# Kernel tuning notes

Measured on AMD Instinct MI355X. Metric: run time of the kernel, lower is better.

## Reference

```python
import jax, jax.numpy as jnp
import numpy as np

N_NODES = 20000
IN_CH = 7
HID = 256
HEADS = 8
NEG_SLOPE = 0.2


def glorot(key, shape):
    fan = shape[0] + shape[-1] if len(shape) == 2 else int(np.prod(shape))
    lim = jnp.sqrt(6.0 / fan)
    return jax.random.uniform(key, shape, jnp.float32, -lim, lim)


def setup_inputs() -> dict:
    key = jax.random.key(0)
    ks = jax.random.split(key, 12)
    x = jax.random.normal(ks[0], (N_NODES, IN_CH), jnp.float32)
    edge_index = jax.random.randint(ks[1], (2, 160000), 0, N_NODES, jnp.int64)
    # conv1: in=7 -> heads=8, out=256, concat
    W1 = glorot(ks[2], (IN_CH, HEADS * HID))
    att_src1 = glorot(ks[3], (HEADS, HID))
    att_dst1 = glorot(ks[4], (HEADS, HID))
    b1 = jnp.zeros((HEADS * HID,), jnp.float32)
    # conv2: in=2048 -> heads=1, out=256, mean (concat=False)
    W2 = glorot(ks[5], (HEADS * HID, 1 * HID))
    att_src2 = glorot(ks[6], (1, HID))
    att_dst2 = glorot(ks[7], (1, HID))
    b2 = jnp.zeros((HID,), jnp.float32)
    return {"x": x, "edge_index": edge_index, "W1": W1, "att_src1": att_src1,
            "att_dst1": att_dst1, "b1": b1, "W2": W2, "att_src2": att_src2,
            "att_dst2": att_dst2, "b2": b2}


def gat_conv(x, src, dst, W, att_src, att_dst, bias, concat):
    # PyG GATConv (eval mode, dropout disabled)
    H, C = att_src.shape
    n = x.shape[0]
    h = (x @ W).reshape(n, H, C)                      # [N,H,C]
    a_src = jnp.sum(h * att_src[None], axis=-1)       # [N,H]
    a_dst = jnp.sum(h * att_dst[None], axis=-1)       # [N,H]
    alpha = a_src[src] + a_dst[dst]                   # [E,H]
    alpha = jax.nn.leaky_relu(alpha, NEG_SLOPE)
    # segment softmax over incoming edges of each destination node
    amax = jax.ops.segment_max(alpha, dst, num_segments=n)
    alpha = jnp.exp(alpha - amax[dst])
    denom = jax.ops.segment_sum(alpha, dst, num_segments=n)
    alpha = alpha / (denom[dst] + 1e-16)
    msg = h[src] * alpha[:, :, None]                  # [E,H,C] gather + weight
    out = jax.ops.segment_sum(msg, dst, num_segments=n)  # scatter-add aggregate
    out = out.reshape(n, H * C) if concat else out.mean(axis=1)
    return out + bias


def reference(x, edge_index, W1, att_src1, att_dst1, b1, W2, att_src2, att_dst2, b2):
    n = x.shape[0]
    # PyG GATConv default: add self-loops
    loops = jnp.arange(n, dtype=edge_index.dtype)
    src = jnp.concatenate([edge_index[0], loops])
    dst = jnp.concatenate([edge_index[1], loops])
    h = gat_conv(x, src, dst, W1, att_src1, att_dst1, b1, concat=True)
    h = jax.nn.elu(h)
    out = gat_conv(h, src, dst, W2, att_src2, att_dst2, b2, concat=False)
    return out
```

## Files before the change

kernel.cpp:

```cpp
#include <hip/hip_runtime.h>
#include <hip/hip_bf16.h>

#define N_NODES 20000
#define E_ORIG  160000
#define E_TOT   180000
#define HEADS   8
#define HID     256
#define F1      2048
#define NEG     0.2f
#define MAXDEG  96
#define GBKS    32

typedef __attribute__((ext_vector_type(8))) short  short8;
typedef __attribute__((ext_vector_type(4))) short  short4_;
typedef __attribute__((ext_vector_type(4))) float  f32x4;
typedef __attribute__((ext_vector_type(2))) float  f32x2;

__device__ inline float bf2f(ushort u){ union{unsigned u32; float f;} v; v.u32=((unsigned)u)<<16; return v.f; }
__device__ inline ushort f2bf(float f){
  union{float f; unsigned u;} v; v.f=f;
  unsigned lsb=(v.u>>16)&1u; v.u += 0x7fffu + lsb; return (ushort)(v.u>>16);
}

__device__ inline void gload16(const ushort* g, ushort* s){
  __builtin_amdgcn_global_load_lds((const __attribute__((address_space(1))) unsigned int*)g,
                                   (__attribute__((address_space(3))) unsigned int*)s, 16, 0, 0);
}

__global__ __launch_bounds__(256) void k_pre(const float* __restrict__ x, const float* __restrict__ W1,
    const float* __restrict__ as1, const float* __restrict__ ad1, const float* __restrict__ W2,
    float* __restrict__ a_src1, float* __restrict__ a_dst1, ushort* __restrict__ W2bT,
    int* __restrict__ cnt){
  __shared__ float s_w[128];
  __shared__ ushort sh[256][65];
  int tid = threadIdx.x, bid = blockIdx.x;
  if (tid < 128){
    int t = tid & 63;
    int k = t>>3, i = t&7;
    float v = 0.f;
    if (i < 7){
      const float* wp = W1 + i*F1 + (k<<8);
      const float* ap = ((tid<64) ? as1 : ad1) + (k<<8);
      f32x4 a4 = {0,0,0,0};
      for (int c=0;c<256;c+=4)
        a4 += (*(const f32x4*)&wp[c]) * (*(const f32x4*)&ap[c]);
      v = a4[0]+a4[1]+a4[2]+a4[3];
    }
    s_w[tid] = v;
  }
  __syncthreads();
  {
    int nl = tid>>3, k = tid&7;
    int n = bid*32 + nl;
    if (n < N_NODES){
      float s=0.f, d=0.f;
      const float* ws = &s_w[k*8];
      const float* wd = &s_w[64+k*8];
#pragma unroll
      for (int i=0;i<7;i++){
        float xv = x[n*7+i];
        s += xv*ws[i]; d += xv*wd[i];
      }
      a_src1[n*8+k]=s; a_dst1[n*8+k]=d;
    }
  }
  if (bid >= 32 && bid < 111){
    int i = (bid-32)*256 + tid;
    if (i < N_NODES) cnt[i] = 0;
  }
  if (bid < 32){
    int k0 = bid*64;
    for (int kk=0; kk<64; kk++) sh[tid][kk] = f2bf(W2[(size_t)(k0+kk)*256 + tid]);
    __syncthreads();
#pragma unroll
    for (int c8=0; c8<8; c8++){
      short8 v;
#pragma unroll
      for (int j=0;j<8;j++) v[j] = (short)sh[tid][c8*8+j];
      *(short8*)&W2bT[(size_t)tid*F1 + k0 + c8*8] = v;
    }
  }
}

__global__ void k_scat(const int* __restrict__ ei, int* __restrict__ cnt, int* __restrict__ bucket){
  int e = blockIdx.x*256 + threadIdx.x;
  if (e >= E_TOT) return;
  int s, d;
  if (e < E_ORIG){ s = ei[e]; d = ei[E_ORIG + e]; }
  else           { s = d = e - E_ORIG; }
  int pos = atomicAdd(&cnt[d], 1);
  if (pos < MAXDEG) bucket[d*MAXDEG + pos] = s;
}

__global__ __launch_bounds__(512) void k_sa1(const int* __restrict__ cnt, const int* __restrict__ bucket,
    const float* __restrict__ a_src1, const float* __restrict__ a_dst1,
    const float* __restrict__ x, const float* __restrict__ W1, const float* __restrict__ b1,
    ushort* __restrict__ x2){
  __shared__ float sxa[8][64];
  int tid = threadIdx.x, wv = tid>>6, lane = tid&63;
  int n = blockIdx.x*8 + wv;
  {
    int k = lane>>3, i = lane&7;
    int ie = (i==7)?0:i;
    int base = n*MAXDEG;
    int deg  = cnt[n]; if (deg>MAXDEG) deg=MAXDEG;
    float ad = a_dst1[n*8+k];
    int src0 = (lane<deg)    ? bucket[base+lane]    : 0;
    int src1 = (lane+64<deg) ? bucket[base+lane+64] : 0;
    float denom = 0.f, acc = 0.f;
    int j = 0;
    for (; j+2<=deg; j+=2){
      int s0 = (j<64)   ? __shfl(src0,j)     : __shfl(src1,j-64);
      int s1 = (j+1<64) ? __shfl(src0,j+1)   : __shfl(src1,j-63);
      float A0 = a_src1[(size_t)s0*8+k] + ad;
      float A1 = a_src1[(size_t)s1*8+k] + ad;
      float X0 = x[(size_t)s0*7+ie];
      float X1 = x[(size_t)s1*7+ie];
      A0 = (A0>0.f)?A0:NEG*A0;  A1 = (A1>0.f)?A1:NEG*A1;
      float w0 = __expf(A0),   w1 = __expf(A1);
      denom += w0; acc += w0*X0;
      denom += w1; acc += w1*X1;
    }
    if (j<deg){
      int s0 = (j<64) ? __shfl(src0,j) : __shfl(src1,j-64);
      float A0 = a_src1[(size_t)s0*8+k] + ad;
      A0 = (A0>0.f)?A0:NEG*A0;
      float w0 = __expf(A0);
      denom += w0; acc += w0*x[(size_t)s0*7+ie];
    }
    sxa[wv][lane] = acc/denom;
  }
  __syncthreads();
  int kh = tid>>6, c4 = (tid&63)<<2;
  f32x4 w1r[7];
#pragma unroll
  for (int i=0;i<7;i++) w1r[i] = *(const f32x4*)(W1 + i*F1 + (kh<<8) + c4);
  f32x4 bb = *(const f32x4*)(b1 + (kh<<8) + c4);
#pragma unroll
  for (int g=0; g<8; g++){
    int nn = blockIdx.x*8 + g;
    const float* xa = &sxa[g][kh<<3];
    f32x4 h = bb;
#pragma unroll
    for (int i=0;i<7;i++) h += xa[i]*w1r[i];
    short4_ o;
#pragma unroll
    for (int j=0;j<4;j++){ float v=h[j]; v=(v>0.f)?v:(__expf(v)-1.f); o[j]=(short)f2bf(v); }
    *(short4_*)(x2 + (size_t)nn*F1 + (kh<<8) + c4) = o;
  }
}

__global__ __launch_bounds__(256,3) void k_gemm2m(const ushort* __restrict__ A,
    const ushort* __restrict__ BT, ushort* __restrict__ h2b,
    const float* __restrict__ as2, const float* __restrict__ ad2,
    float* __restrict__ asrc_p, float* __restrict__ adst_p){
  __shared__ __align__(16) ushort S[2][(64+128)*64];
  int tid = threadIdx.x, bid = blockIdx.x;
  int m0 = (bid>>1)*64, n0 = (bid&1)*128, nb = bid&1;
  int w = tid>>6, l = tid&63;
  int lrow = l&15, lk = l>>4;
  int nc = w<<5;

  const ushort* gp[6];
#pragma unroll
  for (int rep=0;rep<6;rep++){
    int lin = rep*256 + tid;
    if (lin < 512){
      int r = lin>>3, s = lin&7;
      int grow = m0 + r; if (grow >= N_NODES) grow = N_NODES-1;
      gp[rep] = A + (size_t)grow*F1 + ((s ^ (r&7))<<3);
    } else {
      int j = lin - 512;
      int c = j>>3, s = j&7;
      gp[rep] = BT + (size_t)(n0+c)*F1 + ((s ^ (c&7))<<3);
    }
  }

  f32x4 acc[4][2] = {};

#pragma unroll
  for (int rep=0;rep<6;rep++) gload16(gp[rep], &S[0][(rep*256+tid)<<3]);
  __syncthreads();

  int cur = 0;
  for (int t=0; t<GBKS; t++){
    if (t+1 < GBKS){
      int k0 = (t+1)<<6;
#pragma unroll
      for (int rep=0;rep<6;rep++) gload16(gp[rep]+k0, &S[cur^1][(rep*256+tid)<<3]);
    }
    const ushort* as_ = &S[cur][0];
    const ushort* bs_ = &S[cur][4096];
#pragma unroll
    for (int kk=0;kk<2;kk++){
      short8 af[4], bfr[2];
#pragma unroll
      for (int m=0;m<4;m++){
        int r = (m<<4) + lrow;
        af[m] = *(const short8*)&as_[(r<<6) + ((((kk<<2)|lk) ^ (r&7))<<3)];
      }
#pragma unroll
      for (int n=0;n<2;n++){
        int c = nc + (n<<4) + lrow;
        bfr[n] = *(const short8*)&bs_[(c<<6) + ((((kk<<2)|lk) ^ (c&7))<<3)];
      }
#pragma unroll
      for (int m=0;m<4;m++)
#pragma unroll
        for (int n=0;n<2;n++)
          acc[m][n] = __builtin_amdgcn_mfma_f32_16x16x32_bf16(af[m], bfr[n], acc[m][n], 0,0,0);
    }
    __syncthreads();
    cur ^= 1;
  }

  float* sps = (float*)&S[0][0];
  float* spd = sps + 256;
  float s2v[2], d2v[2];
#pragma unroll
  for (int n=0;n<2;n++){
    int col = n0 + nc + (n<<4) + lrow;
    s2v[n]=as2[col]; d2v[n]=ad2[col];
  }
#pragma unroll
  for (int m=0;m<4;m++){
#pragma unroll
    for (int j=0;j<4;j++){
      int lr = (m<<4) + (lk<<2) + j;
      int grow = m0 + lr;
      bool ok = grow < N_NODES;
      float ps=0.f, pd=0.f;
#pragma unroll
      for (int n=0;n<2;n++){
        float v = acc[m][n][j];
        ps += v*s2v[n]; pd += v*d2v[n];
        if (ok) h2b[(size_t)grow*256 + n0 + nc+(n<<4)+lrow] = f2bf(v);
      }
      ps += __shfl_xor(ps,8); ps += __shfl_xor(ps,4); ps += __shfl_xor(ps,2); ps += __shfl_xor(ps,1);
      pd += __shfl_xor(pd,8); pd += __shfl_xor(pd,4); pd += __shfl_xor(pd,2); pd += __shfl_xor(pd,1);
      if (lrow==0){
        sps[(lr<<2) | w] = ps;
        spd[(lr<<2) | w] = pd;
      }
    }
  }
  __syncthreads();
  if (tid < 64){
    int grow = m0 + tid;
    if (grow < N_NODES){
      f32x4 a = *(const f32x4*)&sps[tid<<2];
      f32x4 b = *(const f32x4*)&spd[tid<<2];
      asrc_p[(size_t)grow*2 + nb] = a[0]+a[1]+a[2]+a[3];
      adst_p[(size_t)grow*2 + nb] = b[0]+b[1]+b[2]+b[3];
    }
  }
}

__global__ __launch_bounds__(256) void k_agg2(const int* __restrict__ cnt, const int* __restrict__ bucket,
    const float* __restrict__ asrc_p, const float* __restrict__ adst_p, const ushort* __restrict__ h2b,
    const float* __restrict__ b2, float* __restrict__ out){
  int tid = threadIdx.x, wv = tid>>6, lane = tid&63;
  int n = blockIdx.x*4 + wv;
  int base = n*MAXDEG;
  int deg  = cnt[n]; if (deg > MAXDEG) deg = MAXDEG;
  f32x2 adp = *(const f32x2*)(adst_p + (size_t)n*2);
  float ad = adp[0] + adp[1];

  int src0 = (lane<deg)     ? bucket[base+lane]    : 0;
  int src1 = (lane+64<deg)  ? bucket[base+lane+64] : 0;
  float a0 = -1e30f, a1 = -1e30f;
  if (lane<deg)   { f32x2 sp = *(const f32x2*)(asrc_p + (size_t)src0*2);
                    float a = sp[0]+sp[1]+ad; a0 = (a>0.f)?a:NEG*a; }
  if (lane+64<deg){ f32x2 sp = *(const f32x2*)(asrc_p + (size_t)src1*2);
                    float a = sp[0]+sp[1]+ad; a1 = (a>0.f)?a:NEG*a; }
  float m = fmaxf(a0,a1);
  for (int off=32; off; off>>=1) m = fmaxf(m, __shfl_xor(m,off));
  float e0 = (lane<deg)    ? __expf(a0-m) : 0.f;
  float e1 = (lane+64<deg) ? __expf(a1-m) : 0.f;
  float s = e0+e1;
  for (int off=32; off; off>>=1) s += __shfl_xor(s,off);
  float inv = 1.f/(s+1e-16f);
  e0 *= inv; e1 *= inv;

  int c0 = lane<<2;
  float acc0=0.f, acc1=0.f, acc2=0.f, acc3=0.f;
  int d1 = (deg<64)?deg:64;
  for (int j=0;j<d1;j++){
    float w = __shfl(e0, j);
    int  sj = __shfl(src0, j);
    short4_ hv = *(const short4_*)(h2b + (size_t)sj*256 + c0);
    acc0 += w*bf2f((ushort)hv[0]); acc1 += w*bf2f((ushort)hv[1]);
    acc2 += w*bf2f((ushort)hv[2]); acc3 += w*bf2f((ushort)hv[3]);
  }
  for (int j=64;j<deg;j++){
    float w = __shfl(e1, j-64);
    int  sj = __shfl(src1, j-64);
    short4_ hv = *(const short4_*)(h2b + (size_t)sj*256 + c0);
    acc0 += w*bf2f((ushort)hv[0]); acc1 += w*bf2f((ushort)hv[1]);
    acc2 += w*bf2f((ushort)hv[2]); acc3 += w*bf2f((ushort)hv[3]);
  }
  f32x4 bb = *(const f32x4*)(b2 + c0);
  f32x4 o; o[0]=acc0+bb[0]; o[1]=acc1+bb[1]; o[2]=acc2+bb[2]; o[3]=acc3+bb[3];
  *(f32x4*)(out + (size_t)n*256 + c0) = o;
}

extern "C" void kernel_launch(void* const* d_in, const int* in_sizes, int n_in,
                              void* d_out, int out_size, void* d_ws, size_t ws_size,
                              hipStream_t stream){
  const float* x      = (const float*)d_in[0];
  const int*   ei     = (const int*)  d_in[1];
  const float* W1     = (const float*)d_in[2];
  const float* att_s1 = (const float*)d_in[3];
  const float* att_d1 = (const float*)d_in[4];
  const float* b1     = (const float*)d_in[5];
  const float* W2     = (const float*)d_in[6];
  const float* att_s2 = (const float*)d_in[7];
  const float* att_d2 = (const float*)d_in[8];
  const float* b2     = (const float*)d_in[9];
  float* out = (float*)d_out;

  char* p = (char*)d_ws;
  auto alloc = [&](size_t bytes)->char*{ char* r = p; p += (bytes + 255) & ~(size_t)255; return r; };
  ushort* x2    = (ushort*)alloc((size_t)N_NODES*F1*2);
  ushort* W2bT  = (ushort*)alloc((size_t)F1*256*2);
  ushort* h2b   = (ushort*)alloc((size_t)N_NODES*256*2);
  float*  a_src1= (float*) alloc((size_t)N_NODES*8*4);
  float*  a_dst1= (float*) alloc((size_t)N_NODES*8*4);
  float*  asrc_p= (float*) alloc((size_t)N_NODES*2*4);
  float*  adst_p= (float*) alloc((size_t)N_NODES*2*4);
  int*    cnt   = (int*)   alloc((size_t)N_NODES*4);
  int*    bucket= (int*)   alloc((size_t)N_NODES*MAXDEG*4);

  k_pre    <<<(N_NODES+31)/32, 256, 0, stream>>>(x, W1, att_s1, att_d1, W2,
                                                 a_src1, a_dst1, W2bT, cnt);
  k_scat   <<<(E_TOT+255)/256, 256, 0, stream>>>(ei, cnt, bucket);
  k_sa1    <<<N_NODES/8, 512, 0, stream>>>(cnt, bucket, a_src1, a_dst1, x, W1, b1, x2);
  k_gemm2m <<<((N_NODES+63)/64)*2, 256, 0, stream>>>(x2, W2bT, h2b, att_s2, att_d2, asrc_p, adst_p);
  k_agg2   <<<N_NODES/4, 256, 0, stream>>>(cnt, bucket, asrc_p, adst_p, h2b, b2, out);
}
```

Before: 121.1 us.

## Fuse all GAT stages into one persistent cooperative kernel with grid syncs

Replaces the five separate launches with a single cooperative kernel of 512 persistent blocks that runs preprocessing, edge bucketing, layer-1 aggregation, the layer-2 GEMM and layer-2 aggregation in sequence, separated by grid-wide barriers. This removes per-launch overhead and the gaps between kernels. The GEMM stage changes tiling to 80-row tiles so 500 blocks cover the nodes. In exchange, work-per-block loops and grid syncs may reduce occupancy and load balance compared with the larger grids used before. The multi-kernel path is kept as a fallback if the cooperative launch fails.

After: 420.4 us. 3.47x slower.

```diff
diff --git a/kernel.cpp b/kernel.cpp
--- a/kernel.cpp
+++ b/kernel.cpp
@@ -1,5 +1,8 @@
 #include <hip/hip_runtime.h>
 #include <hip/hip_bf16.h>
+#include <hip/hip_cooperative_groups.h>
+
+namespace cg = cooperative_groups;
 
 #define N_NODES 20000
 #define E_ORIG  160000
@@ -10,6 +13,7 @@
 #define NEG     0.2f
 #define MAXDEG  96
 #define GBKS    32
+#define GRID    512
 
 typedef __attribute__((ext_vector_type(8))) short  short8;
 typedef __attribute__((ext_vector_type(4))) short  short4_;
@@ -25,6 +29,296 @@
 __device__ inline void gload16(const ushort* g, ushort* s){
   __builtin_amdgcn_global_load_lds((const __attribute__((address_space(1))) unsigned int*)g,
                                    (__attribute__((address_space(3))) unsigned int*)s, 16, 0, 0);
+}
+
+struct GP {
+  const float *x; const int *ei;
+  const float *W1, *as1, *ad1, *b1, *W2, *as2, *ad2, *b2;
+  float *out;
+  ushort *x2, *W2bT, *h2b;
+  float *a_src1, *a_dst1, *asrc_p, *adst_p;
+  int *cnt, *bucket;
+};
+
+__global__ __launch_bounds__(256,2) void k_all(GP p){
+  __shared__ __align__(16) char smem[53248];
+  cg::grid_group grid = cg::this_grid();
+  int tid = threadIdx.x, bid = blockIdx.x;
+
+  {
+    float* s_w = (float*)smem;
+    if (tid < 128){
+      int t = tid & 63, k = t>>3, i = t&7;
+      float v = 0.f;
+      if (i < 7){
+        const float* wp = p.W1 + i*F1 + (k<<8);
+        const float* ap = ((tid<64) ? p.as1 : p.ad1) + (k<<8);
+        f32x4 a4 = {0,0,0,0};
+        for (int c=0;c<256;c+=4) a4 += (*(const f32x4*)&wp[c]) * (*(const f32x4*)&ap[c]);
+        v = a4[0]+a4[1]+a4[2]+a4[3];
+      }
+      s_w[tid] = v;
+    }
+    __syncthreads();
+    for (int u=bid; u<625; u+=GRID){
+      int nl = tid>>3, k = tid&7;
+      int n = u*32 + nl;
+      if (n < N_NODES){
+        float s=0.f, d=0.f;
+        const float* ws = &s_w[k*8];
+        const float* wd = &s_w[64+k*8];
+#pragma unroll
+        for (int i=0;i<7;i++){
+          float xv = p.x[n*7+i];
+          s += xv*ws[i]; d += xv*wd[i];
+        }
+        p.a_src1[n*8+k]=s; p.a_dst1[n*8+k]=d;
+      }
+    }
+    for (int i=bid*256+tid; i<N_NODES; i+=GRID*256) p.cnt[i]=0;
+    if (bid < 32){
+      __syncthreads();
+      ushort (*sh)[65] = (ushort(*)[65])(smem + 512);
+      int k0 = bid*64;
+      for (int kk=0; kk<64; kk++) sh[tid][kk] = f2bf(p.W2[(size_t)(k0+kk)*256 + tid]);
+      __syncthreads();
+#pragma unroll
+      for (int c8=0; c8<8; c8++){
+        short8 v;
+#pragma unroll
+        for (int j=0;j<8;j++) v[j] = (short)sh[tid][c8*8+j];
+        *(short8*)&p.W2bT[(size_t)tid*F1 + k0 + c8*8] = v;
+      }
+    }
+  }
+  grid.sync();
+
+  for (int e=bid*256+tid; e<E_TOT; e+=GRID*256){
+    int s, d;
+    if (e < E_ORIG){ s = p.ei[e]; d = p.ei[E_ORIG + e]; }
+    else           { s = d = e - E_ORIG; }
+    int pos = atomicAdd(&p.cnt[d], 1);
+    if (pos < MAXDEG) p.bucket[d*MAXDEG + pos] = s;
+  }
+  grid.sync();
+
+  {
+    float (*sxa)[64] = (float(*)[64])smem;
+    int wv = tid>>6, lane = tid&63;
+    int kh = tid>>5, c0a = (tid&31)<<3;
+    f32x4 w1a[7], w1b[7];
+#pragma unroll
+    for (int i=0;i<7;i++){
+      const float* wp = p.W1 + i*F1 + (kh<<8) + c0a;
+      w1a[i] = *(const f32x4*)wp; w1b[i] = *(const f32x4*)(wp+4);
+    }
+    f32x4 b1a = *(const f32x4*)(p.b1 + (kh<<8) + c0a);
+    f32x4 b1b = *(const f32x4*)(p.b1 + (kh<<8) + c0a + 4);
+    for (int u=bid; u<N_NODES/4; u+=GRID){
+      {
+        int n = u*4 + wv;
+        int k = lane>>3, i = lane&7;
+        int ie = (i==7)?0:i;
+        int base = n*MAXDEG;
+        int deg  = p.cnt[n]; if (deg>MAXDEG) deg=MAXDEG;
+        float ad = p.a_dst1[n*8+k];
+        int src0 = (lane<deg)    ? p.bucket[base+lane]    : 0;
+        int src1 = (lane+64<deg) ? p.bucket[base+lane+64] : 0;
+        float denom = 0.f, acc = 0.f;
+        int j = 0;
+        for (; j+2<=deg; j+=2){
+          int s0 = (j<64)   ? __shfl(src0,j)     : __shfl(src1,j-64);
+          int s1 = (j+1<64) ? __shfl(src0,j+1)   : __shfl(src1,j-63);
+          float A0 = p.a_src1[(size_t)s0*8+k] + ad;
+          float A1 = p.a_src1[(size_t)s1*8+k] + ad;
+          float X0 = p.x[(size_t)s0*7+ie];
+          float X1 = p.x[(size_t)s1*7+ie];
+          A0 = (A0>0.f)?A0:NEG*A0;  A1 = (A1>0.f)?A1:NEG*A1;
+          float w0 = __expf(A0),   w1 = __expf(A1);
+          denom += w0; acc += w0*X0;
+          denom += w1; acc += w1*X1;
+        }
+        if (j<deg){
+          int s0 = (j<64) ? __shfl(src0,j) : __shfl(src1,j-64);
+          float A0 = p.a_src1[(size_t)s0*8+k] + ad;
+          A0 = (A0>0.f)?A0:NEG*A0;
+          float w0 = __expf(A0);
+          denom += w0; acc += w0*p.x[(size_t)s0*7+ie];
+        }
+        sxa[wv][lane] = acc/denom;
+      }
+      __syncthreads();
+#pragma unroll
+      for (int g=0; g<4; g++){
+        int nn = u*4 + g;
+        const float* xa = &sxa[g][kh<<3];
+        f32x4 ha=b1a, hb=b1b;
+#pragma unroll
+        for (int i=0;i<7;i++){
+          float xv = xa[i];
+          ha += xv*w1a[i]; hb += xv*w1b[i];
+        }
+        short8 o;
+#pragma unroll
+        for (int j=0;j<4;j++){ float v=ha[j]; v=(v>0.f)?v:(__expf(v)-1.f); o[j]  =(short)f2bf(v); }
+#pragma unroll
+        for (int j=0;j<4;j++){ float v=hb[j]; v=(v>0.f)?v:(__expf(v)-1.f); o[4+j]=(short)f2bf(v); }
+        *(short8*)(p.x2 + (size_t)nn*F1 + (kh<<8) + c0a) = o;
+      }
+      __syncthreads();
+    }
+  }
+  grid.sync();
+
+  if (bid < 500){
+    ushort* S0 = (ushort*)smem;
+    ushort* Sb[2] = { S0, S0 + 13312 };
+    int m0 = (bid>>1)*80, n0 = (bid&1)*128, nb = bid&1;
+    int w = tid>>6, l = tid&63;
+    int lrow = l&15, lk = l>>4;
+    int nc = w<<5;
+
+    const ushort* gp[7];
+#pragma unroll
+    for (int rep=0;rep<7;rep++){
+      int lin = rep*256 + tid;
+      if (lin < 640){
+        int r = lin>>3, s = lin&7;
+        gp[rep] = p.x2 + (size_t)(m0+r)*F1 + ((s ^ (r&7))<<3);
+      } else if (lin < 1664){
+        int j = lin - 640;
+        int c = j>>3, s = j&7;
+        gp[rep] = p.W2bT + (size_t)(n0+c)*F1 + ((s ^ (c&7))<<3);
+      } else gp[rep] = p.W2bT;
+    }
+
+    f32x4 acc[5][2] = {};
+
+#pragma unroll
+    for (int rep=0;rep<6;rep++) gload16(gp[rep], &Sb[0][(rep*256+tid)<<3]);
+    if (tid < 128) gload16(gp[6], &Sb[0][(6*256+tid)<<3]);
+    __syncthreads();
+
+    int cur = 0;
+    for (int t=0; t<GBKS; t++){
+      if (t+1 < GBKS){
+        int k0 = (t+1)<<6;
+#pragma unroll
+        for (int rep=0;rep<6;rep++) gload16(gp[rep]+k0, &Sb[cur^1][(rep*256+tid)<<3]);
+        if (tid < 128) gload16(gp[6]+k0, &Sb[cur^1][(6*256+tid)<<3]);
+      }
+      const ushort* as_ = Sb[cur];
+      const ushort* bs_ = Sb[cur] + 5120;
+#pragma unroll
+      for (int kk=0;kk<2;kk++){
+        short8 af[5], bfr[2];
+#pragma unroll
+        for (int m=0;m<5;m++){
+          int r = (m<<4) + lrow;
+          af[m] = *(const short8*)&as_[(r<<6) + ((((kk<<2)|lk) ^ (r&7))<<3)];
+        }
+#pragma unroll
+        for (int n=0;n<2;n++){
+          int c = nc + (n<<4) + lrow;
+          bfr[n] = *(const short8*)&bs_[(c<<6) + ((((kk<<2)|lk) ^ (c&7))<<3)];
+        }
+#pragma unroll
+        for (int m=0;m<5;m++)
+#pragma unroll
+          for (int n=0;n<2;n++)
+            acc[m][n] = __builtin_amdgcn_mfma_f32_16x16x32_bf16(af[m], bfr[n], acc[m][n], 0,0,0);
+      }
+      __syncthreads();
+      cur ^= 1;
+    }
+
+    float* sps = (float*)smem;
+    float* spd = sps + 320;
+    float s2v[2], d2v[2];
+#pragma unroll
+    for (int n=0;n<2;n++){
+      int col = n0 + nc + (n<<4) + lrow;
+      s2v[n]=p.as2[col]; d2v[n]=p.ad2[col];
+    }
+#pragma unroll
+    for (int m=0;m<5;m++){
+#pragma unroll
+      for (int j=0;j<4;j++){
+        int lr = (m<<4) + (lk<<2) + j;
+        int grow = m0 + lr;
+        float ps=0.f, pd=0.f;
+#pragma unroll
+        for (int n=0;n<2;n++){
+          float v = acc[m][n][j];
+          ps += v*s2v[n]; pd += v*d2v[n];
+          p.h2b[(size_t)grow*256 + n0 + nc+(n<<4)+lrow] = f2bf(v);
+        }
+        ps += __shfl_xor(ps,8); ps += __shfl_xor(ps,4); ps += __shfl_xor(ps,2); ps += __shfl_xor(ps,1);
+        pd += __shfl_xor(pd,8); pd += __shfl_xor(pd,4); pd += __shfl_xor(pd,2); pd += __shfl_xor(pd,1);
+        if (lrow==0){
+          sps[(lr<<2) | w] = ps;
+          spd[(lr<<2) | w] = pd;
+        }
+      }
+    }
+    __syncthreads();
+    if (tid < 80){
+      int grow = m0 + tid;
+      f32x4 a = *(const f32x4*)&sps[tid<<2];
+      f32x4 b = *(const f32x4*)&spd[tid<<2];
+      p.asrc_p[(size_t)grow*2 + nb] = a[0]+a[1]+a[2]+a[3];
+      p.adst_p[(size_t)grow*2 + nb] = b[0]+b[1]+b[2]+b[3];
+    }
+  }
+  grid.sync();
+
+  {
+    int wv = tid>>6, lane = tid&63;
+    for (int u=bid; u<N_NODES/4; u+=GRID){
+      int n = u*4 + wv;
+      int base = n*MAXDEG;
+      int deg  = p.cnt[n]; if (deg > MAXDEG) deg = MAXDEG;
+      f32x2 adp = *(const f32x2*)(p.adst_p + (size_t)n*2);
+      float ad = adp[0] + adp[1];
+
+      int src0 = (lane<deg)     ? p.bucket[base+lane]    : 0;
+      int src1 = (lane+64<deg)  ? p.bucket[base+lane+64] : 0;
+      float a0 = -1e30f, a1 = -1e30f;
+      if (lane<deg)   { f32x2 sp = *(const f32x2*)(p.asrc_p + (size_t)src0*2);
+                        float a = sp[0]+sp[1]+ad; a0 = (a>0.f)?a:NEG*a; }
+      if (lane+64<deg){ f32x2 sp = *(const f32x2*)(p.asrc_p + (size_t)src1*2);
+                        float a = sp[0]+sp[1]+ad; a1 = (a>0.f)?a:NEG*a; }
+      float m = fmaxf(a0,a1);
+      for (int off=32; off; off>>=1) m = fmaxf(m, __shfl_xor(m,off));
+      float e0 = (lane<deg)    ? __expf(a0-m) : 0.f;
+      float e1 = (lane+64<deg) ? __expf(a1-m) : 0.f;
+      float s = e0+e1;
+      for (int off=32; off; off>>=1) s += __shfl_xor(s,off);
+      float inv = 1.f/(s+1e-16f);
+      e0 *= inv; e1 *= inv;
+
+      int c0 = lane<<2;
+      float acc0=0.f, acc1=0.f, acc2=0.f, acc3=0.f;
+      int d1 = (deg<64)?deg:64;
+      for (int j=0;j<d1;j++){
+        float w = __shfl(e0, j);
+        int  sj = __shfl(src0, j);
+        short4_ hv = *(const short4_*)(p.h2b + (size_t)sj*256 + c0);
+        acc0 += w*bf2f((ushort)hv[0]); acc1 += w*bf2f((ushort)hv[1]);
+        acc2 += w*bf2f((ushort)hv[2]); acc3 += w*bf2f((ushort)hv[3]);
+      }
+      for (int j=64;j<deg;j++){
+        float w = __shfl(e1, j-64);
+        int  sj = __shfl(src1, j-64);
+        short4_ hv = *(const short4_*)(p.h2b + (size_t)sj*256 + c0);
+        acc0 += w*bf2f((ushort)hv[0]); acc1 += w*bf2f((ushort)hv[1]);
+        acc2 += w*bf2f((ushort)hv[2]); acc3 += w*bf2f((ushort)hv[3]);
+      }
+      f32x4 bb = *(const f32x4*)(p.b2 + c0);
+      f32x4 o; o[0]=acc0+bb[0]; o[1]=acc1+bb[1]; o[2]=acc2+bb[2]; o[3]=acc3+bb[3];
+      *(f32x4*)(p.out + (size_t)n*256 + c0) = o;
+    }
+  }
 }
 
 __global__ __launch_bounds__(256) void k_pre(const float* __restrict__ x, const float* __restrict__ W1,
@@ -307,34 +601,43 @@
 extern "C" void kernel_launch(void* const* d_in, const int* in_sizes, int n_in,
                               void* d_out, int out_size, void* d_ws, size_t ws_size,
                               hipStream_t stream){
-  const float* x      = (const float*)d_in[0];
-  const int*   ei     = (const int*)  d_in[1];
-  const float* W1     = (const float*)d_in[2];
-  const float* att_s1 = (const float*)d_in[3];
-  const float* att_d1 = (const float*)d_in[4];
-  const float* b1     = (const float*)d_in[5];
-  const float* W2     = (const float*)d_in[6];
-  const float* att_s2 = (const float*)d_in[7];
-  const float* att_d2 = (const float*)d_in[8];
-  const float* b2     = (const float*)d_in[9];
-  float* out = (float*)d_out;
-
-  char* p = (char*)d_ws;
-  auto alloc = [&](size_t bytes)->char*{ char* r = p; p += (bytes + 255) & ~(size_t)255; return r; };
-  ushort* x2    = (ushort*)alloc((size_t)N_NODES*F1*2);
-  ushort* W2bT  = (ushort*)alloc((size_t)F1*256*2);
-  ushort* h2b   = (ushort*)alloc((size_t)N_NODES*256*2);
-  float*  a_src1= (float*) alloc((size_t)N_NODES*8*4);
-  float*  a_dst1= (float*) alloc((size_t)N_NODES*8*4);
-  float*  asrc_p= (float*) alloc((size_t)N_NODES*2*4);
-  float*  adst_p= (float*) alloc((size_t)N_NODES*2*4);
-  int*    cnt   = (int*)   alloc((size_t)N_NODES*4);
-  int*    bucket= (int*)   alloc((size_t)N_NODES*MAXDEG*4);
-
-  k_pre    <<<(N_NODES+31)/32, 256, 0, stream>>>(x, W1, att_s1, att_d1, W2,
-                                                 a_src1, a_dst1, W2bT, cnt);
-  k_scat   <<<(E_TOT+255)/256, 256, 0, stream>>>(ei, cnt, bucket);
-  k_sa1    <<<N_NODES/8, 512, 0, stream>>>(cnt, bucket, a_src1, a_dst1, x, W1, b1, x2);
-  k_gemm2m <<<((N_NODES+63)/64)*2, 256, 0, stream>>>(x2, W2bT, h2b, att_s2, att_d2, asrc_p, adst_p);
-  k_agg2   <<<N_NODES/4, 256, 0, stream>>>(cnt, bucket, asrc_p, adst_p, h2b, b2, out);
-}
+  GP p;
+  p.x      = (const float*)d_in[0];
+  p.ei     = (const int*)  d_in[1];
+  p.W1     = (const float*)d_in[2];
+  p.as1    = (const float*)d_in[3];
+  p.ad1    = (const float*)d_in[4];
+  p.b1     = (const float*)d_in[5];
+  p.W2     = (const float*)d_in[6];
+  p.as2    = (const float*)d_in[7];
+  p.ad2    = (const float*)d_in[8];
+  p.b2     = (const float*)d_in[9];
+  p.out    = (float*)d_out;
+
+  char* q = (char*)d_ws;
+  auto alloc = [&](size_t bytes)->char*{ char* r = q; q += (bytes + 255) & ~(size_t)255; return r; };
+  p.x2     = (ushort*)alloc((size_t)N_NODES*F1*2);
+  p.W2bT   = (ushort*)alloc((size_t)F1*256*2);
+  p.h2b    = (ushort*)alloc((size_t)N_NODES*256*2);
+  p.a_src1 = (float*) alloc((size_t)N_NODES*8*4);
+  p.a_dst1 = (float*) alloc((size_t)N_NODES*8*4);
+  p.asrc_p = (float*) alloc((size_t)N_NODES*2*4);
+  p.adst_p = (float*) alloc((size_t)N_NODES*2*4);
+  p.cnt    = (int*)   alloc((size_t)N_NODES*4);
+  p.bucket = (int*)   alloc((size_t)N_NODES*MAXDEG*4);
+
+  void* args[] = { (void*)&p };
+  hipError_t err = hipLaunchCooperativeKernel((const void*)k_all, dim3(GRID), dim3(256),
+                                              args, 0, stream);
+  if (err != hipSuccess){
+    k_pre   <<<(N_NODES+31)/32, 256, 0, stream>>>(p.x, p.W1, p.as1, p.ad1, p.W2,
+                                                  p.a_src1, p.a_dst1, p.W2bT, p.cnt);
+    k_scat  <<<(E_TOT+255)/256, 256, 0, stream>>>(p.ei, p.cnt, p.bucket);
+    k_sa1   <<<N_NODES/8, 512, 0, stream>>>(p.cnt, p.bucket, p.a_src1, p.a_dst1,
+                                            p.x, p.W1, p.b1, p.x2);
+    k_gemm2m<<<((N_NODES+63)/64)*2, 256, 0, stream>>>(p.x2, p.W2bT, p.h2b,
+                                                      p.as2, p.ad2, p.asrc_p, p.adst_p);
+    k_agg2  <<<N_NODES/4, 256, 0, stream>>>(p.cnt, p.bucket, p.asrc_p, p.adst_p,
+                                            p.h2b, p.b2, p.out);
+  }
+}
```
